# Optimization experiments

Measured on AMD Instinct MI355X. Metric: run time of the kernel, lower is better.

## Reference

```python
import jax, jax.numpy as jnp
import numpy as np

N = 100000   # nodes
E = 3200000  # directed edges
F = 16       # num_features (colors)


def setup_inputs() -> dict:
    key = jax.random.key(0)
    ks = jax.random.split(key, 5)
    x = jax.random.normal(ks[0], (N, F), dtype=jnp.float32)
    edge_index = jax.random.randint(ks[1], (2, E), 0, N)
    # Glorot-ish scaled weights for the 5 identical blocks (F->64->32->F)
    W1 = jax.random.normal(ks[2], (5, F, 64), dtype=jnp.float32) * (1.0 / np.sqrt(F))
    W2 = jax.random.normal(ks[3], (5, 64, 32), dtype=jnp.float32) * (1.0 / np.sqrt(64))
    W3 = jax.random.normal(ks[4], (5, 32, F), dtype=jnp.float32) * (1.0 / np.sqrt(32))
    b1 = jnp.zeros((5, 64), dtype=jnp.float32)
    b2 = jnp.zeros((5, 32), dtype=jnp.float32)
    b3 = jnp.zeros((5, F), dtype=jnp.float32)
    return {"x": x, "edge_index": edge_index,
            "W1": W1, "b1": b1, "W2": W2, "b2": b2, "W3": W3, "b3": b3}


def _gcn(x, W, b, src, dst, norm, n):
    # GCNConv: project, then symmetric-normalized neighbor sum (self-loops in src/dst)
    h = x @ W                                   # [n, d_out]
    msg = h[src] * norm[:, None]                # [e+n, d_out] gather + scale
    out = jax.ops.segment_sum(msg, dst, num_segments=n)
    return out + b


def reference(x, edge_index, W1, b1, W2, b2, W3, b3):
    n = x.shape[0]
    loops = jnp.arange(n)
    src = jnp.concatenate([edge_index[0], loops])  # add self loops (PyG default)
    dst = jnp.concatenate([edge_index[1], loops])
    deg = jax.ops.segment_sum(jnp.ones(src.shape[0], jnp.float32), dst, num_segments=n)
    dis = jax.lax.rsqrt(jnp.maximum(deg, 1.0))     # deg >= 1 due to self loops
    norm = dis[src] * dis[dst]
    for i in range(5):
        x = jax.nn.relu(_gcn(x, W1[i], b1[i], src, dst, norm, n))
        x = jax.nn.relu(_gcn(x, W2[i], b2[i], src, dst, norm, n))
        x = jax.nn.softmax(_gcn(x, W3[i], b3[i], src, dst, norm, n), axis=1)
    return x
```

## Files before the change

kernel.cpp:

```cpp
#include <hip/hip_runtime.h>

#define NN 100000
#define NE 3200000
#define SLAB 80
#define SLAB4 (SLAB / 4)
#define NB 196
#define BSH 9
#define BCAP 20480
#define NBB 500
#define EPB 6400
#define CAP 64

typedef int      vi4 __attribute__((ext_vector_type(4)));
typedef float    vf4 __attribute__((ext_vector_type(4)));
typedef _Float16 vh8 __attribute__((ext_vector_type(8)));


__global__ __launch_bounds__(512)
void k_bucket(const int* __restrict__ src, const int* __restrict__ dst,
              int* __restrict__ gcur, int* __restrict__ entries) {
    __shared__ int stage[NB * CAP];
    __shared__ int sfill[NB];
    __shared__ int sbase[NB];
    int tid = threadIdx.x;
    for (int i = tid; i < NB; i += 512) sfill[i] = 0;
    __syncthreads();

    int e0 = blockIdx.x * EPB;
    const vi4* d4 = (const vi4*)(dst + e0);
    const vi4* s4 = (const vi4*)(src + e0);
    for (int i = tid; i < EPB / 4; i += 512) {
        vi4 dv = __builtin_nontemporal_load(d4 + i);
        vi4 sv = __builtin_nontemporal_load(s4 + i);
        #pragma unroll
        for (int j = 0; j < 4; j++) {
            int d = dv[j];
            int b = d >> BSH;
            int v = sv[j] | ((d & 511) << 17);
            int p = atomicAdd(&sfill[b], 1);
            if (p < CAP) {
                stage[b * CAP + p] = v;
            } else {
                int gp = atomicAdd(&gcur[b], 1);
                if (gp < BCAP) entries[b * BCAP + gp] = v;
            }
        }
    }
    __syncthreads();

    if (tid < NB) {
        int cnt = min(sfill[tid], CAP);
        sbase[tid] = atomicAdd(&gcur[tid], cnt);
    }
    __syncthreads();

    int wid = tid >> 6, lane = tid & 63;
    for (int b = wid; b < NB; b += 8) {
        int cnt = min(sfill[b], CAP);
        int gbase = sbase[b];
        for (int j = lane; j < cnt; j += 64) {
            int pos = gbase + j;
            if (pos < BCAP)
                __builtin_nontemporal_store(stage[b * CAP + j], entries + b * BCAP + pos);
        }
    }
}

__global__ __launch_bounds__(512)
void k_csr(const int* __restrict__ gcur, const int* __restrict__ entries,
           int* __restrict__ col, int* __restrict__ cnt4, float* __restrict__ dis,
           const float* __restrict__ x, vh8* __restrict__ xs8,
           vh8* __restrict__ h3s8, vh8* __restrict__ h2s8) {
    __shared__ int lcur[512];
    int tid = threadIdx.x;
    int b = blockIdx.x;
    lcur[tid] = 0;
    __syncthreads();
    int nE = min(gcur[b], BCAP);
    const int* ep = entries + b * BCAP;
    int nbase = b << BSH;
    for (int e = tid; e < nE; e += 512) {
        int v = __builtin_nontemporal_load(ep + e);
        int s = v & 0x1FFFF;
        int local = v >> 17;
        int p = atomicAdd(&lcur[local], 1);
        if (p < SLAB) col[(size_t)(nbase + local) * SLAB + p] = s;
    }
    __syncthreads();
    {
        int node = nbase + tid;
        if (node < NN) {
            int c = lcur[tid];
            float dn = rsqrtf((float)(c + 1));
            dis[node] = dn;
            int cc = min(c, SLAB);
            int c4 = (cc + 3) >> 2;
            cnt4[node] = c4;
            int* slab = col + (size_t)node * SLAB;
            for (int k = cc; k < c4 * 4; k++) slab[k] = NN;
            const vf4* xr = (const vf4*)(x + (size_t)node * 16);
            vh8 o0, o1;
            #pragma unroll
            for (int i = 0; i < 4; i++) {
                o0[i]     = (_Float16)(xr[0][i] * dn);
                o0[i + 4] = (_Float16)(xr[1][i] * dn);
                o1[i]     = (_Float16)(xr[2][i] * dn);
                o1[i + 4] = (_Float16)(xr[3][i] * dn);
            }
            xs8[(size_t)node * 2 + 0] = o0;
            xs8[(size_t)node * 2 + 1] = o1;
        }
    }
    if (b == 0 && tid < 8) {
        vh8 z = {(_Float16)0.f, (_Float16)0.f, (_Float16)0.f, (_Float16)0.f,
                 (_Float16)0.f, (_Float16)0.f, (_Float16)0.f, (_Float16)0.f};
        if (tid < 2)      xs8[NN * 2 + tid] = z;
        else if (tid < 4) h3s8[NN * 2 + (tid - 2)] = z;
        else              h2s8[NN * 4 + (tid - 4)] = z;
    }
}

template<int CH, int UNROLL>
__device__ inline void gather4w(const vh8* __restrict__ in, const int4* __restrict__ cp,
                                int c4, int node, int d, int h, float* acc) {
    vh8 self = in[node * CH + d];
    #pragma unroll
    for (int i = 0; i < 8; i++) acc[i] = h ? 0.f : (float)self[i];
    #pragma unroll UNROLL
    for (int k = h; k < c4; k += 4) {
        vi4 cs = __builtin_nontemporal_load((const vi4*)(cp + k));
        vh8 a = in[cs.x * CH + d];
        vh8 b = in[cs.y * CH + d];
        vh8 c = in[cs.z * CH + d];
        vh8 e = in[cs.w * CH + d];
        #pragma unroll
        for (int i = 0; i < 8; i++)
            acc[i] += ((float)a[i] + (float)b[i]) + ((float)c[i] + (float)e[i]);
    }
    #pragma unroll
    for (int i = 0; i < 8; i++) acc[i] += __shfl_xor(acc[i], 1);
    #pragma unroll
    for (int i = 0; i < 8; i++) acc[i] += __shfl_xor(acc[i], 2);
}


__global__ __launch_bounds__(256)
void k_layerA(const vh8* __restrict__ xs, const int* __restrict__ cnt4,
              const int4* __restrict__ colv, const float* __restrict__ dis,
              const float* __restrict__ W1, const float* __restrict__ b1,
              const float* __restrict__ W2, _Float16* __restrict__ h2s) {
    __shared__ float sW1[16 * 64];
    __shared__ float sW2[64 * 32];
    __shared__ float sb1[64];
    __shared__ float st[32 * 16];
    __shared__ _Float16 sx1h[32 * 72];
    int tid = threadIdx.x;
    for (int i = tid; i < 16 * 64; i += 256) sW1[i] = W1[i];
    for (int i = tid; i < 64 * 32; i += 256) sW2[i] = W2[i];
    if (tid < 64) sb1[tid] = b1[tid];

    int nl = tid >> 3, ll = tid & 7, d = ll >> 2, h = ll & 3;
    int node = blockIdx.x * 32 + nl;
    float dn = dis[node];
    float acc[8];
    gather4w<2, 2>(xs, colv + (size_t)node * SLAB4, cnt4[node], node, d, h, acc);
    if (h == 0) {
        vf4 v0 = {acc[0] * dn, acc[1] * dn, acc[2] * dn, acc[3] * dn};
        vf4 v1 = {acc[4] * dn, acc[5] * dn, acc[6] * dn, acc[7] * dn};
        ((vf4*)st)[nl * 4 + d * 2 + 0] = v0;
        ((vf4*)st)[nl * 4 + d * 2 + 1] = v1;
    }
    __syncthreads();

    int c = tid & 63, g = tid >> 6;
    #pragma unroll
    for (int p = 0; p < 2; p++) {
        int nb = g * 8 + p * 4;
        float a0 = sb1[c], a1 = a0, a2 = a0, a3 = a0;
        #pragma unroll
        for (int k = 0; k < 16; k++) {
            float w = sW1[k * 64 + c];
            a0 += st[(nb + 0) * 16 + k] * w;
            a1 += st[(nb + 1) * 16 + k] * w;
            a2 += st[(nb + 2) * 16 + k] * w;
            a3 += st[(nb + 3) * 16 + k] * w;
        }
        sx1h[(nb + 0) * 72 + c] = (_Float16)fmaxf(a0, 0.f);
        sx1h[(nb + 1) * 72 + c] = (_Float16)fmaxf(a1, 0.f);
        sx1h[(nb + 2) * 72 + c] = (_Float16)fmaxf(a2, 0.f);
        sx1h[(nb + 3) * 72 + c] = (_Float16)fmaxf(a3, 0.f);
    }
    __syncthreads();

    int c2 = tid & 31, g2 = tid >> 5;
    #pragma unroll
    for (int p = 0; p < 4; p++) {
        int n2 = g2 * 4 + p;
        const vh8* xr = (const vh8*)(sx1h + n2 * 72);
        float a = 0.f;
        #pragma unroll
        for (int j = 0; j < 8; j++) {
            vh8 v = xr[j];
            #pragma unroll
            for (int i = 0; i < 8; i++)
                a += (float)v[i] * sW2[(j * 8 + i) * 32 + c2];
        }
        int gn = blockIdx.x * 32 + n2;
        h2s[(size_t)gn * 32 + c2] = (_Float16)(a * dis[gn]);
    }
}

__global__ __launch_bounds__(256)
void k_aggmm3(const vh8* __restrict__ h2s, const int* __restrict__ cnt4,
              const int4* __restrict__ colv, const float* __restrict__ dis,
              const float* __restrict__ b2, const float* __restrict__ W3,
              _Float16* __restrict__ h3s) {
    __shared__ float sW[32 * 16];
    __shared__ float sb[32];
    __shared__ float st[16 * 40];
    int tid = threadIdx.x;
    for (int i = tid; i < 32 * 16; i += 256) sW[i] = W3[i];
    if (tid < 32) sb[tid] = b2[tid];
    __syncthreads();

    int nl = tid >> 4, ll = tid & 15, d = ll >> 2, h = ll & 3;
    int node = blockIdx.x * 16 + nl;
    float dn = dis[node];
    float acc[8];
    gather4w<4, 2>(h2s, colv + (size_t)node * SLAB4, cnt4[node], node, d, h, acc);
    if (h == 0) {
        vf4 v0, v1;
        #pragma unroll
        for (int i = 0; i < 4; i++) {
            v0[i] = fmaxf(acc[i] * dn + sb[d * 8 + i], 0.f);
            v1[i] = fmaxf(acc[i + 4] * dn + sb[d * 8 + 4 + i], 0.f);
        }
        vf4* sp = (vf4*)(st + nl * 40 + d * 8);
        sp[0] = v0;
        sp[1] = v1;
    }
    __syncthreads();

    int c = tid & 15, n = tid >> 4;
    float a0 = 0.f;
    #pragma unroll
    for (int k = 0; k < 32; k++) a0 += st[n * 40 + k] * sW[k * 16 + c];
    int gn = blockIdx.x * 16 + n;
    h3s[(size_t)gn * 16 + c] = (_Float16)(a0 * dis[gn]);
}

__global__ __launch_bounds__(256)
void k_agg_soft(const vh8* __restrict__ in, const int* __restrict__ cnt4,
                const int4* __restrict__ colv, const float* __restrict__ dis,
                const float* __restrict__ bias, float* __restrict__ out,
                vh8* __restrict__ out2) {
    int tid = threadIdx.x;
    int nl = tid >> 3, ll = tid & 7, d = ll >> 2, h = ll & 3;
    int node = blockIdx.x * 32 + nl;
    float dn = dis[node];
    float acc[8];
    gather4w<2, 2>(in, colv + (size_t)node * SLAB4, cnt4[node], node, d, h, acc);
    #pragma unroll
    for (int i = 0; i < 8; i++) acc[i] = acc[i] * dn + bias[d * 8 + i];
    float m = acc[0];
    #pragma unroll
    for (int i = 1; i < 8; i++) m = fmaxf(m, acc[i]);
    m = fmaxf(m, __shfl_xor(m, 4));
    float ev[8], s = 0.f;
    #pragma unroll
    for (int i = 0; i < 8; i++) { ev[i] = __expf(acc[i] - m); s += ev[i]; }
    s += __shfl_xor(s, 4);
    float inv = 1.0f / s;
    if (h == 0) {
        vf4 o0 = {ev[0] * inv, ev[1] * inv, ev[2] * inv, ev[3] * inv};
        vf4 o1 = {ev[4] * inv, ev[5] * inv, ev[6] * inv, ev[7] * inv};
        __builtin_nontemporal_store(o0, (vf4*)out + (size_t)node * 4 + d * 2);
        __builtin_nontemporal_store(o1, (vf4*)out + (size_t)node * 4 + d * 2 + 1);
        vh8 ho;
        #pragma unroll
        for (int i = 0; i < 8; i++) ho[i] = (_Float16)(ev[i] * inv * dn);
        out2[(size_t)node * 2 + d] = ho;
    }
}


static inline size_t align_up(size_t v, size_t a) { return (v + a - 1) & ~(a - 1); }

extern "C" void kernel_launch(void* const* d_in, const int* in_sizes, int n_in,
                              void* d_out, int out_size, void* d_ws, size_t ws_size,
                              hipStream_t stream) {
    const float* x   = (const float*)d_in[0];
    const int*   ei  = (const int*)d_in[1];
    const float* W1  = (const float*)d_in[2];
    const float* b1  = (const float*)d_in[3];
    const float* W2  = (const float*)d_in[4];
    const float* b2  = (const float*)d_in[5];
    const float* W3  = (const float*)d_in[6];
    const float* b3  = (const float*)d_in[7];
    float* outp = (float*)d_out;

    const int* src = ei;
    const int* dst = ei + NE;

    char* ws = (char*)d_ws;
    size_t off = 0;
    auto carve = [&](size_t bytes) { void* p = ws + off; off = align_up(off + bytes, 256); return p; };
    int*      gcur  = (int*)     carve(NB * 4);
    int*      cnt4  = (int*)     carve(NN * 4);
    float*    dis   = (float*)   carve(NN * 4);
    int*      col   = (int*)     carve((size_t)NN * SLAB * 4);
    _Float16* xs    = (_Float16*)carve((size_t)(NN + 1) * 16 * 2);
    _Float16* h3s   = (_Float16*)carve((size_t)(NN + 1) * 16 * 2);
    int*      entries = (int*)   carve((size_t)NB * BCAP * 4);
    _Float16* h2s   = (_Float16*)carve((size_t)(NN + 1) * 32 * 2);
    (void)ws_size; (void)n_in; (void)in_sizes; (void)out_size;

    hipMemsetAsync(gcur, 0, NB * 4, stream);
    k_bucket<<<NBB, 512, 0, stream>>>(src, dst, gcur, entries);
    k_csr<<<NB, 512, 0, stream>>>(gcur, entries, col, cnt4, dis, x,
                                  (vh8*)xs, (vh8*)h3s, (vh8*)h2s);

    const int gA = NN / 32;
    const int gB = NN / 16;
    const int gC = NN / 32;

    for (int l = 0; l < 5; l++) {
        k_layerA<<<gA, 256, 0, stream>>>((const vh8*)xs, cnt4, (const int4*)col, dis,
                                         W1 + l * 16 * 64, b1 + l * 64, W2 + l * 64 * 32, h2s);
        k_aggmm3<<<gB, 256, 0, stream>>>((const vh8*)h2s, cnt4, (const int4*)col, dis,
                                         b2 + l * 32, W3 + l * 32 * 16, h3s);
        k_agg_soft<<<gC, 256, 0, stream>>>((const vh8*)h3s, cnt4, (const int4*)col, dis,
                                           b3 + l * 16, outp, (vh8*)xs);
    }
}
```

Measured before the change: 678.2 us.

## Async weight loads to LDS, transposed W2, vectorized LDS reads, skip intermediate fp32 output

Weight and bias loads into shared memory now go through global_load_lds (when the compiler supports it) and are issued before the neighbor gather, so they can overlap with it. W2 is stored transposed with a rotation so the second matmul can read weights as float4. Matmul inner loops now read activations and weights from LDS as float4. Launch bounds request 8 blocks per CU, and the softmax kernel writes the fp32 output only on the last layer. Risks: the first __syncthreads after the gather must also cover the async LDS writes, and the occupancy hint may cause register spills.

```diff
diff --git a/kernel.cpp b/kernel.cpp
--- a/kernel.cpp
+++ b/kernel.cpp
@@ -14,6 +14,16 @@
 typedef int      vi4 __attribute__((ext_vector_type(4)));
 typedef float    vf4 __attribute__((ext_vector_type(4)));
 typedef _Float16 vh8 __attribute__((ext_vector_type(8)));
+
+#if __has_builtin(__builtin_amdgcn_global_load_lds)
+#define HAS_GLL 1
+typedef const __attribute__((address_space(1))) void* gas1_t;
+typedef __attribute__((address_space(3))) void* las3_t;
+#define GLL4(g, l)  __builtin_amdgcn_global_load_lds((gas1_t)(g), (las3_t)(l), 4, 0, 0)
+#define GLL16(g, l) __builtin_amdgcn_global_load_lds((gas1_t)(g), (las3_t)(l), 16, 0, 0)
+#else
+#define HAS_GLL 0
+#endif
 
 
 __global__ __launch_bounds__(512)
@@ -144,26 +154,53 @@
 }
 
 
-__global__ __launch_bounds__(256)
+__global__ __launch_bounds__(256, 8)
 void k_layerA(const vh8* __restrict__ xs, const int* __restrict__ cnt4,
               const int4* __restrict__ colv, const float* __restrict__ dis,
               const float* __restrict__ W1, const float* __restrict__ b1,
               const float* __restrict__ W2, _Float16* __restrict__ h2s) {
     __shared__ float sW1[16 * 64];
-    __shared__ float sW2[64 * 32];
+    __shared__ float sW2T[32 * 64];
     __shared__ float sb1[64];
     __shared__ float st[32 * 16];
     __shared__ _Float16 sx1h[32 * 72];
     int tid = threadIdx.x;
-    for (int i = tid; i < 16 * 64; i += 256) sW1[i] = W1[i];
-    for (int i = tid; i < 64 * 32; i += 256) sW2[i] = W2[i];
-    if (tid < 64) sb1[tid] = b1[tid];
+    int wid = tid >> 6, lane = tid & 63;
+
+#if HAS_GLL
+    GLL16(W1 + wid * 256 + lane * 4, sW1 + wid * 256);
+    if (wid == 0) GLL4(b1 + lane, sb1);
+    #pragma unroll
+    for (int r = 0; r < 8; r++) {
+        int cc = r * 4 + wid;
+        int kk = (lane - 4 * cc) & 63;
+        GLL4(W2 + kk * 32 + cc, sW2T + cc * 64);
+    }
+#endif
 
     int nl = tid >> 3, ll = tid & 7, d = ll >> 2, h = ll & 3;
     int node = blockIdx.x * 32 + nl;
     float dn = dis[node];
     float acc[8];
     gather4w<2, 2>(xs, colv + (size_t)node * SLAB4, cnt4[node], node, d, h, acc);
+
+#if !HAS_GLL
+    {
+        vf4 w1r = ((const vf4*)W1)[tid];
+        ((vf4*)sW1)[tid] = w1r;
+        vf4 wa = ((const vf4*)W2)[tid];
+        vf4 wb = ((const vf4*)W2)[tid + 256];
+        #pragma unroll
+        for (int i = 0; i < 4; i++) {
+            int f = tid * 4 + i;
+            sW2T[(f & 31) * 64 + (((f >> 5) + 4 * (f & 31)) & 63)] = wa[i];
+            int g2_ = tid * 4 + 1024 + i;
+            sW2T[(g2_ & 31) * 64 + (((g2_ >> 5) + 4 * (g2_ & 31)) & 63)] = wb[i];
+        }
+        if (tid < 64) sb1[tid] = b1[tid];
+    }
+#endif
+
     if (h == 0) {
         vf4 v0 = {acc[0] * dn, acc[1] * dn, acc[2] * dn, acc[3] * dn};
         vf4 v1 = {acc[4] * dn, acc[5] * dn, acc[6] * dn, acc[7] * dn};
@@ -178,12 +215,16 @@
         int nb = g * 8 + p * 4;
         float a0 = sb1[c], a1 = a0, a2 = a0, a3 = a0;
         #pragma unroll
-        for (int k = 0; k < 16; k++) {
-            float w = sW1[k * 64 + c];
-            a0 += st[(nb + 0) * 16 + k] * w;
-            a1 += st[(nb + 1) * 16 + k] * w;
-            a2 += st[(nb + 2) * 16 + k] * w;
-            a3 += st[(nb + 3) * 16 + k] * w;
+        for (int kq = 0; kq < 4; kq++) {
+            vf4 s0 = *(const vf4*)(st + (nb + 0) * 16 + kq * 4);
+            vf4 s1 = *(const vf4*)(st + (nb + 1) * 16 + kq * 4);
+            vf4 s2 = *(const vf4*)(st + (nb + 2) * 16 + kq * 4);
+            vf4 s3 = *(const vf4*)(st + (nb + 3) * 16 + kq * 4);
+            #pragma unroll
+            for (int i = 0; i < 4; i++) {
+                float w = sW1[(kq * 4 + i) * 64 + c];
+                a0 += s0[i] * w; a1 += s1[i] * w; a2 += s2[i] * w; a3 += s3[i] * w;
+            }
         }
         sx1h[(nb + 0) * 72 + c] = (_Float16)fmaxf(a0, 0.f);
         sx1h[(nb + 1) * 72 + c] = (_Float16)fmaxf(a1, 0.f);
@@ -193,6 +234,7 @@
     __syncthreads();
 
     int c2 = tid & 31, g2 = tid >> 5;
+    const float* wrow = sW2T + c2 * 64;
     #pragma unroll
     for (int p = 0; p < 4; p++) {
         int n2 = g2 * 4 + p;
@@ -201,39 +243,51 @@
         #pragma unroll
         for (int j = 0; j < 8; j++) {
             vh8 v = xr[j];
-            #pragma unroll
-            for (int i = 0; i < 8; i++)
-                a += (float)v[i] * sW2[(j * 8 + i) * 32 + c2];
+            vf4 w0 = *(const vf4*)(wrow + ((8 * j + 4 * c2) & 63));
+            vf4 w1 = *(const vf4*)(wrow + ((8 * j + 4 + 4 * c2) & 63));
+            a += (float)v[0] * w0[0]; a += (float)v[1] * w0[1];
+            a += (float)v[2] * w0[2]; a += (float)v[3] * w0[3];
+            a += (float)v[4] * w1[0]; a += (float)v[5] * w1[1];
+            a += (float)v[6] * w1[2]; a += (float)v[7] * w1[3];
         }
         int gn = blockIdx.x * 32 + n2;
         h2s[(size_t)gn * 32 + c2] = (_Float16)(a * dis[gn]);
     }
 }
 
-__global__ __launch_bounds__(256)
+__global__ __launch_bounds__(256, 8)
 void k_aggmm3(const vh8* __restrict__ h2s, const int* __restrict__ cnt4,
               const int4* __restrict__ colv, const float* __restrict__ dis,
               const float* __restrict__ b2, const float* __restrict__ W3,
               _Float16* __restrict__ h3s) {
     __shared__ float sW[32 * 16];
-    __shared__ float sb[32];
     __shared__ float st[16 * 40];
     int tid = threadIdx.x;
-    for (int i = tid; i < 32 * 16; i += 256) sW[i] = W3[i];
-    if (tid < 32) sb[tid] = b2[tid];
-    __syncthreads();
+    int wid = tid >> 6, lane = tid & 63;
+
+#if HAS_GLL
+    if (wid < 2) GLL16(W3 + wid * 256 + lane * 4, sW + wid * 256);
+#endif
 
     int nl = tid >> 4, ll = tid & 15, d = ll >> 2, h = ll & 3;
     int node = blockIdx.x * 16 + nl;
     float dn = dis[node];
     float acc[8];
     gather4w<4, 2>(h2s, colv + (size_t)node * SLAB4, cnt4[node], node, d, h, acc);
+
+#if !HAS_GLL
+    sW[tid] = W3[tid];
+    sW[tid + 256] = W3[tid + 256];
+#endif
+
     if (h == 0) {
+        vf4 bl = ((const vf4*)b2)[d * 2];
+        vf4 bh = ((const vf4*)b2)[d * 2 + 1];
         vf4 v0, v1;
         #pragma unroll
         for (int i = 0; i < 4; i++) {
-            v0[i] = fmaxf(acc[i] * dn + sb[d * 8 + i], 0.f);
-            v1[i] = fmaxf(acc[i + 4] * dn + sb[d * 8 + 4 + i], 0.f);
+            v0[i] = fmaxf(acc[i] * dn + bl[i], 0.f);
+            v1[i] = fmaxf(acc[i + 4] * dn + bh[i], 0.f);
         }
         vf4* sp = (vf4*)(st + nl * 40 + d * 8);
         sp[0] = v0;
@@ -244,24 +298,31 @@
     int c = tid & 15, n = tid >> 4;
     float a0 = 0.f;
     #pragma unroll
-    for (int k = 0; k < 32; k++) a0 += st[n * 40 + k] * sW[k * 16 + c];
+    for (int kq = 0; kq < 8; kq++) {
+        vf4 s = *(const vf4*)(st + n * 40 + kq * 4);
+        #pragma unroll
+        for (int i = 0; i < 4; i++)
+            a0 += s[i] * sW[(kq * 4 + i) * 16 + c];
+    }
     int gn = blockIdx.x * 16 + n;
     h3s[(size_t)gn * 16 + c] = (_Float16)(a0 * dis[gn]);
 }
 
-__global__ __launch_bounds__(256)
+__global__ __launch_bounds__(256, 8)
 void k_agg_soft(const vh8* __restrict__ in, const int* __restrict__ cnt4,
                 const int4* __restrict__ colv, const float* __restrict__ dis,
                 const float* __restrict__ bias, float* __restrict__ out,
-                vh8* __restrict__ out2) {
+                vh8* __restrict__ out2, int last) {
     int tid = threadIdx.x;
     int nl = tid >> 3, ll = tid & 7, d = ll >> 2, h = ll & 3;
     int node = blockIdx.x * 32 + nl;
     float dn = dis[node];
     float acc[8];
     gather4w<2, 2>(in, colv + (size_t)node * SLAB4, cnt4[node], node, d, h, acc);
-    #pragma unroll
-    for (int i = 0; i < 8; i++) acc[i] = acc[i] * dn + bias[d * 8 + i];
+    vf4 bl = ((const vf4*)bias)[d * 2];
+    vf4 bh = ((const vf4*)bias)[d * 2 + 1];
+    #pragma unroll
+    for (int i = 0; i < 4; i++) { acc[i] = acc[i] * dn + bl[i]; acc[i + 4] = acc[i + 4] * dn + bh[i]; }
     float m = acc[0];
     #pragma unroll
     for (int i = 1; i < 8; i++) m = fmaxf(m, acc[i]);
@@ -272,10 +333,12 @@
     s += __shfl_xor(s, 4);
     float inv = 1.0f / s;
     if (h == 0) {
-        vf4 o0 = {ev[0] * inv, ev[1] * inv, ev[2] * inv, ev[3] * inv};
-        vf4 o1 = {ev[4] * inv, ev[5] * inv, ev[6] * inv, ev[7] * inv};
-        __builtin_nontemporal_store(o0, (vf4*)out + (size_t)node * 4 + d * 2);
-        __builtin_nontemporal_store(o1, (vf4*)out + (size_t)node * 4 + d * 2 + 1);
+        if (last) {
+            vf4 o0 = {ev[0] * inv, ev[1] * inv, ev[2] * inv, ev[3] * inv};
+            vf4 o1 = {ev[4] * inv, ev[5] * inv, ev[6] * inv, ev[7] * inv};
+            __builtin_nontemporal_store(o0, (vf4*)out + (size_t)node * 4 + d * 2);
+            __builtin_nontemporal_store(o1, (vf4*)out + (size_t)node * 4 + d * 2 + 1);
+        }
         vh8 ho;
         #pragma unroll
         for (int i = 0; i < 8; i++) ho[i] = (_Float16)(ev[i] * inv * dn);
@@ -330,6 +393,6 @@
         k_aggmm3<<<gB, 256, 0, stream>>>((const vh8*)h2s, cnt4, (const int4*)col, dis,
                                          b2 + l * 32, W3 + l * 32 * 16, h3s);
         k_agg_soft<<<gC, 256, 0, stream>>>((const vh8*)h3s, cnt4, (const int4*)col, dis,
-                                           b3 + l * 16, outp, (vh8*)xs);
-    }
-}
+                                           b3 + l * 16, outp, (vh8*)xs, l == 4 ? 1 : 0);
+    }
+}
```

New measurement: 676.3 us. About the same (-0.3%).
